# Optimization experiments

Hardware: AMD Instinct MI355X
Metric: run time of the kernel (lower is better)

Reference implementation:

```python
import jax, jax.numpy as jnp
import numpy as np
from jax import lax

V_VOX, T_PTS, D, H, W = 12000, 35, 10, 200, 176
EPS = 1e-5


def _bn(x, g, b, axes, shape):
    m = x.mean(axes, keepdims=True)
    v = x.var(axes, keepdims=True)  # biased var, matches torch BN training stats
    return g.reshape(shape) * (x - m) * lax.rsqrt(v + EPS) + b.reshape(shape)


def _conv3d(x, w, b):
    y = lax.conv_general_dilated(x, w, (1, 1, 1), 'SAME',
                                 dimension_numbers=('NCDHW', 'OIDHW', 'NCDHW'))
    return y + b[None, :, None, None, None]


def _conv2d(x, w, b):
    y = lax.conv_general_dilated(x, w, (1, 1), 'SAME',
                                 dimension_numbers=('NCHW', 'OIHW', 'NCHW'))
    return y + b[None, :, None, None]


def setup_inputs() -> dict:
    key = jax.random.key(0)
    ks = jax.random.split(key, 12)
    voxels = jax.random.normal(ks[0], (1, V_VOX, T_PTS, 4), jnp.float32)
    # unique voxel coordinates (the torch loop overwrites on duplicates; unique avoids ambiguity)
    rng = np.random.default_rng(0)
    flat = rng.choice(D * H * W, size=V_VOX, replace=False)
    z = flat // (H * W); rem = flat % (H * W)
    coords = jnp.asarray(np.stack([z, rem // W, rem % W], axis=1), dtype=jnp.int32)
    s = 0.05
    p = dict(
        w_lin=jax.random.normal(ks[1], (32, 4), jnp.float32) * s,
        b_lin=jnp.zeros((32,), jnp.float32),
        g_bn0=jnp.ones((32,), jnp.float32), be_bn0=jnp.zeros((32,), jnp.float32),
        w_c3a=jax.random.normal(ks[2], (64, 32, 3, 3, 3), jnp.float32) * s,
        b_c3a=jnp.zeros((64,), jnp.float32),
        g_bn1=jnp.ones((64,), jnp.float32), be_bn1=jnp.zeros((64,), jnp.float32),
        w_c3b=jax.random.normal(ks[3], (64, 64, 3, 3, 3), jnp.float32) * s,
        b_c3b=jnp.zeros((64,), jnp.float32),
        g_bn2=jnp.ones((64,), jnp.float32), be_bn2=jnp.zeros((64,), jnp.float32),
        w_r1=jax.random.normal(ks[4], (128, 64, 3, 3), jnp.float32) * s,
        b_r1=jnp.zeros((128,), jnp.float32),
        w_r2=jax.random.normal(ks[5], (8, 128, 1, 1), jnp.float32) * s,
        b_r2=jnp.zeros((8,), jnp.float32),
    )
    return dict(voxels=voxels, coords=coords, **p)


def reference(voxels, coords, w_lin, b_lin, g_bn0, be_bn0,
              w_c3a, b_c3a, g_bn1, be_bn1, w_c3b, b_c3b, g_bn2, be_bn2,
              w_r1, b_r1, w_r2, b_r2):
    B, V, T, C = voxels.shape
    # SimpleVFE: linear -> BN1d (batch stats) -> relu -> max over points
    h = voxels.reshape(B * V * T, C) @ w_lin.T + b_lin          # [BVT,32]
    h = jax.nn.relu(_bn(h, g_bn0, be_bn0, 0, (1, 32)))
    feats = h.reshape(B, V, T, 32).max(axis=2)                  # [B,V,32]
    # fused scatter into dense volume (replaces per-voxel python loop)
    volume = jnp.zeros((B, 32, D, H, W), voxels.dtype)
    volume = volume.at[0, :, coords[:, 0], coords[:, 1], coords[:, 2]].set(feats[0])
    # 3D backbone
    x = jax.nn.relu(_bn(_conv3d(volume, w_c3a, b_c3a), g_bn1, be_bn1, (0, 2, 3, 4), (1, 64, 1, 1, 1)))
    x = jax.nn.relu(_bn(_conv3d(x, w_c3b, b_c3b), g_bn2, be_bn2, (0, 2, 3, 4), (1, 64, 1, 1, 1)))
    x = x.mean(axis=2)                                          # collapse depth -> [B,64,H,W]
    # RPN head
    out = _conv2d(jax.nn.relu(_conv2d(x, w_r1, b_r1)), w_r2, b_r2)  # [B,8,H,W]
    box = jnp.concatenate([out[:, 0:3], jnp.exp(out[:, 3:6]),
                           jnp.tanh(out[:, 6:7]), jax.nn.sigmoid(out[:, 7:8])], axis=1)
    return box
```

## Files before the change

kernel.cpp:

```cpp
#include <hip/hip_runtime.h>
#include <math.h>

#define V_VOX 12000
#define T_PTS 35
#define DD 10
#define HH 200
#define WW 176
#define EPSV 1e-5f

#define DP 12
#define HP 202
#define WP 178
#define PPLN (HP * WP)
#define PVOX (DP * PPLN)
#define NPIX (DD * HH * WW)
#define HWPIX (HH * WW)

typedef _Float16 half_t;
typedef _Float16 f16x8 __attribute__((ext_vector_type(8)));
typedef float f32x4 __attribute__((ext_vector_type(4)));

#define WPA_OFF 0
#define WPB_OFF 110592
#define WPR1_OFF 331776
#define STATS_OFF 479232
#define FEATS_OFF 483328
#define VOLP_OFF 2019328
#define X1P_OFF 29633536
#define Y_OFF 84861952
#define PLANE_OFF 129917952
#define R1OUT_OFF 134520320

#define S_BN0S 0
#define S_BN0Q 32
#define S_BN1S 64
#define S_BN1Q 128
#define S_BN2S 192
#define S_BN2Q 256
#define C0A 320
#define C0B 352
#define C1A 384
#define C1B 448
#define C2A 512
#define C2B 576

__global__ void k_pack(const float* __restrict__ w, half_t* __restrict__ wp,
                       int IC, int NT, int OC) {
    int id = blockIdx.x * 256 + threadIdx.x;
    int OCT = OC >> 4, KH = IC >> 5;
    int total = NT * KH * OCT * 512;
    if (id >= total) return;
    int j = id & 7;
    int lane = (id >> 3) & 63;
    int rest = id >> 9;
    int ot = rest % OCT; rest /= OCT;
    int kh = rest % KH;
    int tap = rest / KH;
    int oc = ot * 16 + (lane & 15);
    int ic = kh * 32 + (lane >> 4) * 8 + j;
    wp[id] = (half_t)w[(oc * IC + ic) * NT + tap];
}

__global__ void k_vfe_stats(const float4* __restrict__ vox, const float* __restrict__ w_lin,
                            const float* __restrict__ b_lin, float* __restrict__ S) {
    int tid = blockIdx.x * 256 + threadIdx.x;
    int c = threadIdx.x & 31;
    float4 w = ((const float4*)w_lin)[c];
    float bl = b_lin[c];
    float s = 0.f, q = 0.f;
    const int np = V_VOX * T_PTS;
    int stride = gridDim.x * 8;
    for (int p = tid >> 5; p < np; p += stride) {
        float4 v = vox[p];
        float d = v.x * w.x + v.y * w.y + v.z * w.z + v.w * w.w + bl;
        s += d;
        q += d * d;
    }
    s += __shfl_xor(s, 32);
    q += __shfl_xor(q, 32);
    if ((threadIdx.x & 63) < 32) {
        atomicAdd(&S[S_BN0S + c], s);
        atomicAdd(&S[S_BN0Q + c], q);
    }
}

__global__ void k_bn_final(const float* __restrict__ ss, const float* __restrict__ sq,
                           const float* __restrict__ g, const float* __restrict__ be,
                           float* __restrict__ ca, float* __restrict__ cb, int C, float invN) {
    int c = threadIdx.x;
    if (c >= C) return;
    float m = ss[c] * invN;
    float v = sq[c] * invN - m * m;
    float a = g[c] * rsqrtf(v + EPSV);
    ca[c] = a;
    cb[c] = be[c] - m * a;
}

__global__ void k_vfe_max(const float4* __restrict__ vox, const float* __restrict__ w_lin,
                          const float* __restrict__ b_lin, const float* __restrict__ ca,
                          const float* __restrict__ cb, float* __restrict__ feats) {
    int id = blockIdx.x * 256 + threadIdx.x;
    if (id >= V_VOX * 32) return;
    int c = id & 31;
    int v = id >> 5;
    float4 w = ((const float4*)w_lin)[c];
    float bl = b_lin[c], A = ca[c], B = cb[c];
    float m = 0.f;
    for (int t = 0; t < T_PTS; t++) {
        float4 p = vox[v * T_PTS + t];
        float d = p.x * w.x + p.y * w.y + p.z * w.z + p.w * w.w + bl;
        m = fmaxf(m, A * d + B);
    }
    feats[id] = m;
}

__global__ void k_scatter(const float* __restrict__ feats, const int* __restrict__ coords,
                          half_t* __restrict__ volp) {
    int id = blockIdx.x * 256 + threadIdx.x;
    if (id >= V_VOX * 32) return;
    int c = id & 31;
    int v = id >> 5;
    int z = coords[v * 3 + 0];
    int y = coords[v * 3 + 1];
    int x = coords[v * 3 + 2];
    volp[(((z + 1) * HP + (y + 1)) * WP + (x + 1)) * 32 + c] = (half_t)feats[id];
}

template <int KH, int DZ, int OCTP, bool RELU, bool STATS>
__global__ __launch_bounds__(256, 3) void k_conv(const half_t* __restrict__ in,
                                                 const half_t* __restrict__ wp,
                                                 const float* __restrict__ bias,
                                                 half_t* __restrict__ out,
                                                 float* __restrict__ ssum,
                                                 float* __restrict__ ssq) {
    constexpr int CIN = KH * 32;
    constexpr int OC = OCTP * 16;
    const int lane = threadIdx.x & 63;
    const int wv = threadIdx.x >> 6;
    const int x0 = blockIdx.x * 16;
    const int y0 = (blockIdx.y * 4 + wv) * 4;
    const int z0 = (DZ == 3) ? blockIdx.z : 0;
    const int ocb = (DZ == 3) ? 0 : blockIdx.z * 4;
    if (y0 >= HH) return;

    const int colc = lane & 15, grp = lane >> 4;
    const size_t rstride = (size_t)WP * CIN;

    f32x4 acc[4][4];
#pragma unroll
    for (int m = 0; m < 4; m++)
#pragma unroll
        for (int n = 0; n < 4; n++) acc[m][n] = (f32x4)(0.f);

#pragma unroll 1
    for (int dz = 0; dz < DZ; ++dz) {
#pragma unroll 1
        for (int dx = 0; dx < 3; ++dx) {
#pragma unroll
            for (int kh = 0; kh < KH; ++kh) {
                const half_t* ib = in + (((size_t)(z0 + dz) * HP + y0) * WP + (x0 + dx)) * CIN
                                   + colc * CIN + kh * 32 + grp * 8;
                f16x8 Af[6];
#pragma unroll
                for (int r = 0; r < 6; ++r) Af[r] = *(const f16x8*)(ib + r * rstride);
                f16x8 Bf[3][4];
#pragma unroll
                for (int dy = 0; dy < 3; ++dy) {
                    const half_t* wb = wp + ((size_t)((dz * 9 + dy * 3 + dx) * KH + kh) * OCTP + ocb) * 512
                                       + lane * 8;
#pragma unroll
                    for (int n = 0; n < 4; ++n) Bf[dy][n] = *(const f16x8*)(wb + n * 512);
                }
#pragma unroll
                for (int dy = 0; dy < 3; ++dy)
#pragma unroll
                    for (int m = 0; m < 4; ++m)
#pragma unroll
                        for (int n = 0; n < 4; ++n)
                            acc[m][n] = __builtin_amdgcn_mfma_f32_16x16x32_f16(
                                Af[dy + m], Bf[dy][n], acc[m][n], 0, 0, 0);
            }
        }
    }

#pragma unroll
    for (int n = 0; n < 4; ++n) {
        int oc = (ocb + n) * 16 + colc;
        float bv = bias[oc];
        float s = 0.f, q = 0.f;
#pragma unroll
        for (int m = 0; m < 4; ++m) {
            int yy = y0 + m;
#pragma unroll
            for (int i = 0; i < 4; ++i) {
                int xx = x0 + grp * 4 + i;
                float v = acc[m][n][i] + bv;
                if (STATS) { s += v; q += v * v; }
                float w = RELU ? fmaxf(v, 0.f) : v;
                out[((size_t)(z0 * HH + yy) * WW + xx) * OC + oc] = (half_t)w;
            }
        }
        if (STATS) {
            s += __shfl_xor(s, 16); s += __shfl_xor(s, 32);
            q += __shfl_xor(q, 16); q += __shfl_xor(q, 32);
            if (lane < 16) {
                atomicAdd(&ssum[oc], s);
                atomicAdd(&ssq[oc], q);
            }
        }
    }
}

__global__ void k_activate(const half_t* __restrict__ y1, const float* __restrict__ ca,
                           const float* __restrict__ cb, half_t* __restrict__ xp) {
    int id = blockIdx.x * 256 + threadIdx.x;
    if (id >= PVOX * 8) return;
    int c0 = (id & 7) * 8;
    int pix = id >> 3;
    int zp = pix / PPLN;
    int rem = pix - zp * PPLN;
    int yp = rem / WP;
    int xq = rem - yp * WP;
    f16x8 o;
    if (zp >= 1 && zp <= DD && yp >= 1 && yp <= HH && xq >= 1 && xq <= WW) {
        size_t p = ((size_t)((zp - 1) * HH + (yp - 1)) * WW + (xq - 1));
        f16x8 v = *(const f16x8*)(y1 + p * 64 + c0);
#pragma unroll
        for (int j = 0; j < 8; j++)
            o[j] = (half_t)fmaxf(ca[c0 + j] * (float)v[j] + cb[c0 + j], 0.f);
    } else {
#pragma unroll
        for (int j = 0; j < 8; j++) o[j] = (half_t)0.f;
    }
    *(f16x8*)(xp + (size_t)pix * 64 + c0) = o;
}

__global__ void k_depthmean(const half_t* __restrict__ y2, const float* __restrict__ ca,
                            const float* __restrict__ cb, half_t* __restrict__ plane) {
    int id = blockIdx.x * 256 + threadIdx.x;
    int c = id & 63;
    int pix = id >> 6;
    int yp = pix / WP;
    int xq = pix - yp * WP;
    float val = 0.f;
    if (yp >= 1 && yp <= HH && xq >= 1 && xq <= WW) {
        float A = ca[c], B = cb[c], s = 0.f;
        const half_t* base = y2 + ((size_t)(yp - 1) * WW + (xq - 1)) * 64 + c;
#pragma unroll
        for (int z = 0; z < DD; z++)
            s += fmaxf(A * (float)base[(size_t)z * HWPIX * 64] + B, 0.f);
        val = s * 0.1f;
    }
    plane[(size_t)pix * 64 + c] = (half_t)val;
}

__global__ void k_r2(const half_t* __restrict__ r1o, const float* __restrict__ w,
                     const float* __restrict__ bias, float* __restrict__ outp) {
    __shared__ float wsm[1024];
    for (int i = threadIdx.x; i < 1024; i += 256) wsm[i] = w[i];
    __syncthreads();
    int p = blockIdx.x * 256 + threadIdx.x;
    if (p >= HWPIX) return;
    float acc[8];
#pragma unroll
    for (int o = 0; o < 8; o++) acc[o] = bias[o];
    const half_t* rb = r1o + (size_t)p * 128;
#pragma unroll 4
    for (int icb = 0; icb < 128; icb += 8) {
        f16x8 v = *(const f16x8*)(rb + icb);
#pragma unroll
        for (int j = 0; j < 8; j++) {
            float vv = (float)v[j];
#pragma unroll
            for (int o = 0; o < 8; o++) acc[o] += vv * wsm[o * 128 + icb + j];
        }
    }
    outp[0 * HWPIX + p] = acc[0];
    outp[1 * HWPIX + p] = acc[1];
    outp[2 * HWPIX + p] = acc[2];
    outp[3 * HWPIX + p] = expf(acc[3]);
    outp[4 * HWPIX + p] = expf(acc[4]);
    outp[5 * HWPIX + p] = expf(acc[5]);
    outp[6 * HWPIX + p] = tanhf(acc[6]);
    outp[7 * HWPIX + p] = 1.f / (1.f + expf(-acc[7]));
}

extern "C" void kernel_launch(void* const* d_in, const int* in_sizes, int n_in,
                              void* d_out, int out_size, void* d_ws, size_t ws_size,
                              hipStream_t stream) {
    const float4* voxels = (const float4*)d_in[0];
    const int* coords = (const int*)d_in[1];
    const float* w_lin = (const float*)d_in[2];
    const float* b_lin = (const float*)d_in[3];
    const float* g_bn0 = (const float*)d_in[4];
    const float* be_bn0 = (const float*)d_in[5];
    const float* w_c3a = (const float*)d_in[6];
    const float* b_c3a = (const float*)d_in[7];
    const float* g_bn1 = (const float*)d_in[8];
    const float* be_bn1 = (const float*)d_in[9];
    const float* w_c3b = (const float*)d_in[10];
    const float* b_c3b = (const float*)d_in[11];
    const float* g_bn2 = (const float*)d_in[12];
    const float* be_bn2 = (const float*)d_in[13];
    const float* w_r1 = (const float*)d_in[14];
    const float* b_r1 = (const float*)d_in[15];
    const float* w_r2 = (const float*)d_in[16];
    const float* b_r2 = (const float*)d_in[17];

    char* ws = (char*)d_ws;
    half_t* wpA = (half_t*)(ws + WPA_OFF);
    half_t* wpB = (half_t*)(ws + WPB_OFF);
    half_t* wpR1 = (half_t*)(ws + WPR1_OFF);
    float* S = (float*)(ws + STATS_OFF);
    float* feats = (float*)(ws + FEATS_OFF);
    half_t* volp = (half_t*)(ws + VOLP_OFF);
    half_t* x1p = (half_t*)(ws + X1P_OFF);
    half_t* Y = (half_t*)(ws + Y_OFF);
    half_t* plane = (half_t*)(ws + PLANE_OFF);
    half_t* r1out = (half_t*)(ws + R1OUT_OFF);
    float* outp = (float*)d_out;

    hipMemsetAsync(S, 0, 320 * sizeof(float), stream);
    hipMemsetAsync(volp, 0, (size_t)PVOX * 32 * sizeof(half_t), stream);

    k_pack<<<216, 256, 0, stream>>>(w_c3a, wpA, 32, 27, 64);
    k_pack<<<432, 256, 0, stream>>>(w_c3b, wpB, 64, 27, 64);
    k_pack<<<288, 256, 0, stream>>>(w_r1, wpR1, 64, 9, 128);

    k_vfe_stats<<<512, 256, 0, stream>>>(voxels, w_lin, b_lin, S);
    k_bn_final<<<1, 64, 0, stream>>>(S + S_BN0S, S + S_BN0Q, g_bn0, be_bn0,
                                     S + C0A, S + C0B, 32, 1.f / 420000.f);
    k_vfe_max<<<1500, 256, 0, stream>>>(voxels, w_lin, b_lin, S + C0A, S + C0B, feats);
    k_scatter<<<1500, 256, 0, stream>>>(feats, coords, volp);

    k_conv<1, 3, 4, false, true><<<dim3(11, 13, 10), 256, 0, stream>>>(
        volp, wpA, b_c3a, Y, S + S_BN1S, S + S_BN1Q);
    k_bn_final<<<1, 64, 0, stream>>>(S + S_BN1S, S + S_BN1Q, g_bn1, be_bn1,
                                     S + C1A, S + C1B, 64, 1.f / 352000.f);
    k_activate<<<13484, 256, 0, stream>>>(Y, S + C1A, S + C1B, x1p);

    k_conv<2, 3, 4, false, true><<<dim3(11, 13, 10), 256, 0, stream>>>(
        x1p, wpB, b_c3b, Y, S + S_BN2S, S + S_BN2Q);
    k_bn_final<<<1, 64, 0, stream>>>(S + S_BN2S, S + S_BN2Q, g_bn2, be_bn2,
                                     S + C2A, S + C2B, 64, 1.f / 352000.f);

    k_depthmean<<<8989, 256, 0, stream>>>(Y, S + C2A, S + C2B, plane);

    k_conv<2, 1, 8, true, false><<<dim3(11, 13, 2), 256, 0, stream>>>(
        plane, wpR1, b_r1, r1out, nullptr, nullptr);
    k_r2<<<138, 256, 0, stream>>>(r1out, w_r2, b_r2, outp);
}
```

Baseline: 540.9 us.

## Stage conv input halo tile in LDS shared across block's waves

Each conv block now cooperatively loads an 18x18 input tile (with channel padding to avoid bank conflicts) into shared memory per depth slice. The four waves then read their A fragments from LDS instead of issuing overlapping global loads. Launch bounds are raised to 4 blocks per CU. The change adds two barriers per depth iteration and uses LDS that could limit occupancy. It also clamps out-of-range rows at the padded edge.

```diff
diff --git a/kernel.cpp b/kernel.cpp
--- a/kernel.cpp
+++ b/kernel.cpp
@@ -126,25 +126,29 @@
     volp[(((z + 1) * HP + (y + 1)) * WP + (x + 1)) * 32 + c] = (half_t)feats[id];
 }
 
-template <int KH, int DZ, int OCTP, bool RELU, bool STATS>
-__global__ __launch_bounds__(256, 3) void k_conv(const half_t* __restrict__ in,
+template <int KH, int CLDS, int DZ, int OCTP, bool RELU, bool STATS>
+__global__ __launch_bounds__(256, 4) void k_conv(const half_t* __restrict__ in,
                                                  const half_t* __restrict__ wp,
                                                  const float* __restrict__ bias,
                                                  half_t* __restrict__ out,
                                                  float* __restrict__ ssum,
                                                  float* __restrict__ ssq) {
     constexpr int CIN = KH * 32;
+    constexpr int C8 = KH * 4;
+    constexpr int TOT8 = 18 * 18 * C8;
     constexpr int OC = OCTP * 16;
-    const int lane = threadIdx.x & 63;
-    const int wv = threadIdx.x >> 6;
+    __shared__ half_t tile[18 * 18 * CLDS];
+
+    const int tid = threadIdx.x;
+    const int lane = tid & 63;
+    const int wv = tid >> 6;
     const int x0 = blockIdx.x * 16;
-    const int y0 = (blockIdx.y * 4 + wv) * 4;
+    const int y0b = blockIdx.y * 16;
     const int z0 = (DZ == 3) ? blockIdx.z : 0;
     const int ocb = (DZ == 3) ? 0 : blockIdx.z * 4;
-    if (y0 >= HH) return;
-
+    const int y0w = y0b + wv * 4;
+    const bool valid = (y0w < HH);
     const int colc = lane & 15, grp = lane >> 4;
-    const size_t rstride = (size_t)WP * CIN;
 
     f32x4 acc[4][4];
 #pragma unroll
@@ -154,35 +158,56 @@
 
 #pragma unroll 1
     for (int dz = 0; dz < DZ; ++dz) {
+        const half_t* sl = in + (size_t)(z0 + dz) * (DZ == 3 ? (size_t)HP * WP * CIN : 0);
+#pragma unroll
+        for (int it = 0; it < (TOT8 + 255) / 256; ++it) {
+            int e = it * 256 + tid;
+            if (e < TOT8) {
+                int ch8 = e % C8;
+                int pxr = e / C8;
+                int px = pxr % 18;
+                int row = pxr / 18;
+                int srow = y0b + row;
+                if (srow > HP - 1) srow = HP - 1;
+                const half_t* s = sl + ((size_t)srow * WP + x0 + px) * CIN + ch8 * 8;
+                *(f16x8*)&tile[pxr * CLDS + ch8 * 8] = *(const f16x8*)s;
+            }
+        }
+        __syncthreads();
+
+        if (valid) {
 #pragma unroll 1
-        for (int dx = 0; dx < 3; ++dx) {
-#pragma unroll
-            for (int kh = 0; kh < KH; ++kh) {
-                const half_t* ib = in + (((size_t)(z0 + dz) * HP + y0) * WP + (x0 + dx)) * CIN
-                                   + colc * CIN + kh * 32 + grp * 8;
-                f16x8 Af[6];
-#pragma unroll
-                for (int r = 0; r < 6; ++r) Af[r] = *(const f16x8*)(ib + r * rstride);
-                f16x8 Bf[3][4];
-#pragma unroll
-                for (int dy = 0; dy < 3; ++dy) {
-                    const half_t* wb = wp + ((size_t)((dz * 9 + dy * 3 + dx) * KH + kh) * OCTP + ocb) * 512
-                                       + lane * 8;
-#pragma unroll
-                    for (int n = 0; n < 4; ++n) Bf[dy][n] = *(const f16x8*)(wb + n * 512);
+            for (int dx = 0; dx < 3; ++dx) {
+#pragma unroll
+                for (int kh = 0; kh < KH; ++kh) {
+                    f16x8 Af[6];
+#pragma unroll
+                    for (int r = 0; r < 6; ++r)
+                        Af[r] = *(const f16x8*)&tile[((wv * 4 + r) * 18 + colc + dx) * CLDS
+                                                     + kh * 32 + grp * 8];
+                    f16x8 Bf[3][4];
+#pragma unroll
+                    for (int dy = 0; dy < 3; ++dy) {
+                        const half_t* wb = wp + ((size_t)((dz * 9 + dy * 3 + dx) * KH + kh) * OCTP
+                                                 + ocb) * 512 + lane * 8;
+#pragma unroll
+                        for (int n = 0; n < 4; ++n) Bf[dy][n] = *(const f16x8*)(wb + n * 512);
+                    }
+#pragma unroll
+                    for (int dy = 0; dy < 3; ++dy)
+#pragma unroll
+                        for (int m = 0; m < 4; ++m)
+#pragma unroll
+                            for (int n = 0; n < 4; ++n)
+                                acc[m][n] = __builtin_amdgcn_mfma_f32_16x16x32_f16(
+                                    Af[dy + m], Bf[dy][n], acc[m][n], 0, 0, 0);
                 }
-#pragma unroll
-                for (int dy = 0; dy < 3; ++dy)
-#pragma unroll
-                    for (int m = 0; m < 4; ++m)
-#pragma unroll
-                        for (int n = 0; n < 4; ++n)
-                            acc[m][n] = __builtin_amdgcn_mfma_f32_16x16x32_f16(
-                                Af[dy + m], Bf[dy][n], acc[m][n], 0, 0, 0);
             }
         }
-    }
-
+        __syncthreads();
+    }
+
+    if (!valid) return;
 #pragma unroll
     for (int n = 0; n < 4; ++n) {
         int oc = (ocb + n) * 16 + colc;
@@ -190,7 +215,7 @@
         float s = 0.f, q = 0.f;
 #pragma unroll
         for (int m = 0; m < 4; ++m) {
-            int yy = y0 + m;
+            int yy = y0w + m;
 #pragma unroll
             for (int i = 0; i < 4; ++i) {
                 int xx = x0 + grp * 4 + i;
@@ -333,20 +358,20 @@
     k_vfe_max<<<1500, 256, 0, stream>>>(voxels, w_lin, b_lin, S + C0A, S + C0B, feats);
     k_scatter<<<1500, 256, 0, stream>>>(feats, coords, volp);
 
-    k_conv<1, 3, 4, false, true><<<dim3(11, 13, 10), 256, 0, stream>>>(
+    k_conv<1, 40, 3, 4, false, true><<<dim3(11, 13, 10), 256, 0, stream>>>(
         volp, wpA, b_c3a, Y, S + S_BN1S, S + S_BN1Q);
     k_bn_final<<<1, 64, 0, stream>>>(S + S_BN1S, S + S_BN1Q, g_bn1, be_bn1,
                                      S + C1A, S + C1B, 64, 1.f / 352000.f);
     k_activate<<<13484, 256, 0, stream>>>(Y, S + C1A, S + C1B, x1p);
 
-    k_conv<2, 3, 4, false, true><<<dim3(11, 13, 10), 256, 0, stream>>>(
+    k_conv<2, 72, 3, 4, false, true><<<dim3(11, 13, 10), 256, 0, stream>>>(
         x1p, wpB, b_c3b, Y, S + S_BN2S, S + S_BN2Q);
     k_bn_final<<<1, 64, 0, stream>>>(S + S_BN2S, S + S_BN2Q, g_bn2, be_bn2,
                                      S + C2A, S + C2B, 64, 1.f / 352000.f);
 
     k_depthmean<<<8989, 256, 0, stream>>>(Y, S + C2A, S + C2B, plane);
 
-    k_conv<2, 1, 8, true, false><<<dim3(11, 13, 2), 256, 0, stream>>>(
+    k_conv<2, 72, 1, 8, true, false><<<dim3(11, 13, 2), 256, 0, stream>>>(
         plane, wpR1, b_r1, r1out, nullptr, nullptr);
     k_r2<<<138, 256, 0, stream>>>(r1out, w_r2, b_r2, outp);
 }
```

Result: faster. 512.4 us (-5.3%).
